# Kernel optimization log

Hardware: AMD Instinct MI355X
Metric: run time of the kernel (lower is better)

Reference implementation:

```python
import jax, jax.numpy as jnp
import numpy as np

H = 512      # config.hidden_dim
N = 64       # batch
W = 512      # sentence length
K = 8        # decode steps = pointer_answers.size(1)
NEG_BIG = 1e10


def setup_inputs() -> dict:
    key = jax.random.key(0)
    ks = jax.random.split(key, 10)
    stdv = 1.0 / np.sqrt(H)
    u = lambda k_, shape, s: jax.random.uniform(k_, shape, jnp.float32, -s, s)
    return {
        "context": jax.random.normal(ks[0], (N, W, 2 * H), jnp.float32),
        "sentence_lens": jax.random.randint(ks[1], (N,), 1, W + 1),
        "pointer_answers": jax.random.randint(ks[2], (N, K), 0, W + 1),
        "V_w": u(ks[3], (H, 2 * H), 1.0 / np.sqrt(2 * H)),
        "W_w": u(ks[4], (H, H), stdv),
        "v": u(ks[5], (H,), stdv),
        "w_ih": u(ks[6], (3 * H, 2 * H), stdv),
        "w_hh": u(ks[7], (3 * H, H), stdv),
        "b_ih": u(ks[8], (3 * H,), stdv),
        "b_hh": u(ks[9], (3 * H,), stdv),
    }


def reference(context, sentence_lens, pointer_answers, V_w, W_w, v, w_ih, w_hh, b_ih, b_hh):
    n, w_len, two_h = context.shape
    h_dim = two_h // 2
    k = pointer_answers.shape[1]

    # encoder output permuted to (W, N, 2H)
    ctx = jnp.swapaxes(context, 0, 1)
    # faithful reproduction of: context_new[i] = (1 - (i >= lens+1)*1e10) * context[i]
    pos = jnp.arange(w_len)[:, None]                                  # (W, 1)
    factor = 1.0 - (pos >= sentence_lens[None, :] + 1).astype(context.dtype) * NEG_BIG  # (W, N)
    ctx_masked = ctx * factor[:, :, None]                             # (W, N, 2H)
    # appended zeros row -> (W+1, N, 2H)
    context_new = jnp.concatenate([ctx_masked, jnp.zeros((1, n, two_h), context.dtype)], axis=0)

    ctx_t = jnp.einsum('snd,hd->snh', context_new, V_w)               # (W+1, N, H) = V(context_new)

    h0 = jnp.zeros((n, h_dim), context.dtype)

    def step(h, _):
        f = jnp.tanh(ctx_t + (h @ W_w.T)[None])                       # (W+1, N, H)
        scores = jnp.einsum('snh,h->sn', f, v)                        # (W+1, N)
        beta = jax.nn.softmax(scores, axis=0)                         # softmax over positions
        aligned = jnp.einsum('sn,snd->nd', beta, context_new)         # (N, 2H)
        # torch GRUCell math
        gi = aligned @ w_ih.T + b_ih                                  # (N, 3H)
        gh = h @ w_hh.T + b_hh                                        # (N, 3H)
        ir, iz, inew = jnp.split(gi, 3, axis=1)
        hr, hz, hnew = jnp.split(gh, 3, axis=1)
        r = jax.nn.sigmoid(ir + hr)
        z = jax.nn.sigmoid(iz + hz)
        ncand = jnp.tanh(inew + r * hnew)
        h_new = (1.0 - z) * ncand + z * h
        return h_new, beta.T                                          # (N, W+1)

    _, betas = jax.lax.scan(step, h0, None, length=k)                 # (k, N, W+1)
    # torch: cat over steps then permute -> (N, k, W+1) -> (N*k, W+1)
    out = jnp.transpose(betas, (1, 0, 2)).reshape(n * k, w_len + 1)
    return out
```

## Files before the change

### kernel.cpp

```cpp
#include <hip/hip_runtime.h>

#define N_    64
#define W_    512
#define H_    512
#define S_    513
#define TWOH_ 1024
#define KS_   8
#define FIXCAP_ 131072

typedef short s16x8 __attribute__((ext_vector_type(8)));
typedef float f32x4 __attribute__((ext_vector_type(4)));
typedef _Float16 h16x8 __attribute__((ext_vector_type(8)));
typedef _Float16 h16x4 __attribute__((ext_vector_type(4)));

__device__ __forceinline__ float tanh_fast(float x) {
  float xc = fminf(fmaxf(x, -15.0f), 15.0f);
  float e = __expf(2.0f * xc);
  return (e - 1.0f) / (e + 1.0f);
}
__device__ __forceinline__ float sigmoid_f(float x) {
  return 1.0f / (1.0f + __expf(-x));
}
__device__ __forceinline__ float wred_sum(float v) {
#pragma unroll
  for (int m = 32; m > 0; m >>= 1) v += __shfl_xor(v, m, 64);
  return v;
}
__device__ __forceinline__ float bf2f(unsigned short u) {
  return __uint_as_float(((unsigned)u) << 16);
}

__device__ __forceinline__ void gld_lds16(const void* g, void* s) {
  __builtin_amdgcn_global_load_lds((__attribute__((address_space(1))) void*)g,
                                   (__attribute__((address_space(3))) void*)s,
                                   16, 0, 0);
}

__global__ __launch_bounds__(256) void k_cvt2(
    const float4* __restrict__ xa, unsigned short* __restrict__ Ahi,
    unsigned short* __restrict__ Alo, const float4* __restrict__ xb,
    unsigned short* __restrict__ Bhi, unsigned short* __restrict__ Blo,
    const float4* __restrict__ xw, _Float16* __restrict__ W16) {
  const int NA = 8388608;
  const int NB = 131072;
  const int NW = 65536;
  const int NT = NA + NB + NW;
  for (int i = blockIdx.x * 256 + threadIdx.x; i < NT; i += gridDim.x * 256) {
    if (i < NA + NB) {
      bool isA = (i < NA);
      float4 v = isA ? xa[i] : xb[i - NA];
      float vs[4] = {v.x, v.y, v.z, v.w};
      unsigned short hb[4], lb[4];
#pragma unroll
      for (int j = 0; j < 4; ++j) {
        unsigned u = __float_as_uint(vs[j]);
        unsigned short h = (unsigned short)((u + 0x7FFFu + ((u >> 16) & 1u)) >> 16);
        float hf = __uint_as_float((unsigned)h << 16);
        float lf = vs[j] - hf;
        unsigned u2 = __float_as_uint(lf);
        unsigned short l = (unsigned short)((u2 + 0x7FFFu + ((u2 >> 16) & 1u)) >> 16);
        hb[j] = h; lb[j] = l;
      }
      ushort4 h4; h4.x = hb[0]; h4.y = hb[1]; h4.z = hb[2]; h4.w = hb[3];
      ushort4 l4; l4.x = lb[0]; l4.y = lb[1]; l4.z = lb[2]; l4.w = lb[3];
      if (isA) {
        ((ushort4*)Ahi)[i] = h4;
        ((ushort4*)Alo)[i] = l4;
      } else {
        ((ushort4*)Bhi)[i - NA] = h4;
        ((ushort4*)Blo)[i - NA] = l4;
      }
    } else {
      int j = i - NA - NB;
      float4 v = xw[j];
      h16x4 o;
      o[0] = (_Float16)v.x; o[1] = (_Float16)v.y;
      o[2] = (_Float16)v.z; o[3] = (_Float16)v.w;
      *(h16x4*)(W16 + (size_t)4 * j) = o;
    }
  }
}

__global__ __launch_bounds__(256, 2) void mfma_gemm(
    const unsigned short* __restrict__ Ahi, const unsigned short* __restrict__ Alo,
    const unsigned short* __restrict__ Bhi, const unsigned short* __restrict__ Blo,
    _Float16* __restrict__ C) {
  __shared__ unsigned short sAh[4096], sAl[4096], sBh[4096], sBl[4096];
  int bid = blockIdx.x;
  int swz = (bid & 7) * 128 + (bid >> 3);
  int mt = swz >> 2, nt = swz & 3;
  int m0 = mt * 128, n0 = nt * 128;
  int tid = threadIdx.x;
  int wave = tid >> 6, lane = tid & 63;
  int wr = wave >> 1, wc = wave & 1;
  int fr = lane & 15, fq = lane >> 4;
  int rA = tid >> 2;
  int cA = (tid & 3) * 8;

  f32x4 acc[4][4] = {};

  const size_t a_row0 = (size_t)(m0 + rA) << 10;
  const size_t a_row1 = (size_t)(m0 + rA + 64) << 10;
  const size_t b_row0 = (size_t)(n0 + rA) << 10;
  const size_t b_row1 = (size_t)(n0 + rA + 64) << 10;
  const int wofs = wave << 9;

  for (int k0 = 0; k0 < 1024; k0 += 32) {
    int off = k0 + cA;
    gld_lds16(Ahi + a_row0 + off, sAh + wofs);
    gld_lds16(Ahi + a_row1 + off, sAh + 2048 + wofs);
    gld_lds16(Alo + a_row0 + off, sAl + wofs);
    gld_lds16(Alo + a_row1 + off, sAl + 2048 + wofs);
    gld_lds16(Bhi + b_row0 + off, sBh + wofs);
    gld_lds16(Bhi + b_row1 + off, sBh + 2048 + wofs);
    gld_lds16(Blo + b_row0 + off, sBl + wofs);
    gld_lds16(Blo + b_row1 + off, sBl + 2048 + wofs);
    __syncthreads();
    s16x8 ah[4], av[4], bh[4], bv[4];
#pragma unroll
    for (int m = 0; m < 4; ++m) {
      int ar = (wr * 64 + m * 16 + fr) * 32 + fq * 8;
      ah[m] = *(const s16x8*)(sAh + ar);
      av[m] = *(const s16x8*)(sAl + ar);
    }
#pragma unroll
    for (int n = 0; n < 4; ++n) {
      int br = (wc * 64 + n * 16 + fr) * 32 + fq * 8;
      bh[n] = *(const s16x8*)(sBh + br);
      bv[n] = *(const s16x8*)(sBl + br);
    }
#pragma unroll
    for (int m = 0; m < 4; ++m)
#pragma unroll
      for (int n = 0; n < 4; ++n) {
        acc[m][n] = __builtin_amdgcn_mfma_f32_16x16x32_bf16(ah[m], bh[n], acc[m][n], 0, 0, 0);
        acc[m][n] = __builtin_amdgcn_mfma_f32_16x16x32_bf16(ah[m], bv[n], acc[m][n], 0, 0, 0);
        acc[m][n] = __builtin_amdgcn_mfma_f32_16x16x32_bf16(av[m], bh[n], acc[m][n], 0, 0, 0);
      }
    __syncthreads();
  }
#pragma unroll
  for (int m = 0; m < 4; ++m) {
    int gr0 = m0 + wr * 64 + m * 16 + fq * 4;
#pragma unroll
    for (int n = 0; n < 4; ++n) {
      int gc = n0 + wc * 64 + n * 16 + fr;
      _Float16* cp = C + (size_t)gr0 * 512 + gc;
#pragma unroll
      for (int r = 0; r < 4; ++r) cp[(size_t)r * 512] = (_Float16)acc[m][n][r];
    }
  }
}

__global__ __launch_bounds__(1024) void k_mscore(
    const int* __restrict__ slens, const float* __restrict__ vvec,
    const _Float16* __restrict__ Vc16, float* __restrict__ scores,
    int* __restrict__ fixcnt, int* __restrict__ fixlist) {
  int nb = blockIdx.x & 63, cb = blockIdx.x >> 6;
  int t = threadIdx.x;
  int len = slens[nb];
  int w = t >> 6, lane = t & 63;
  int hb = lane << 3;
  float4 v0 = *(const float4*)(vvec + hb);
  float4 v1 = *(const float4*)(vvec + hb + 4);
  float vv[8] = {v0.x, v0.y, v0.z, v0.w, v1.x, v1.y, v1.z, v1.w};
  int s0 = max(cb * 128, len + 1);
  int s_end = min((cb + 1) * 128, W_);
  for (int s = s0 + w; s < s_end; s += 16) {
    h16x8 x8 = *(const h16x8*)(Vc16 + ((size_t)nb * W_ + s) * H_ + hb);
    float acc = 0.0f;
#pragma unroll
    for (int i = 0; i < 8; ++i) {
      float vcv = (float)x8[i];
      if (fabsf(vcv) < 6e-5f) {
        int idx = atomicAdd(fixcnt, 1);
        if (idx < FIXCAP_) fixlist[idx] = (nb << 20) | (s << 10) | (hb + i);
      } else {
        acc += (vcv > 0.0f) ? -vv[i] : vv[i];
      }
    }
    acc = wred_sum(acc);
    if (lane == 0) scores[nb * S_ + s] = acc;
  }
}

__global__ __launch_bounds__(256) void k_fix(
    const float* __restrict__ ctx, const float* __restrict__ Vw,
    const float* __restrict__ vvec, const int* __restrict__ fixcnt,
    const int* __restrict__ fixlist, float* __restrict__ scores) {
  int wid = (blockIdx.x * 256 + threadIdx.x) >> 6;
  int lane = threadIdx.x & 63;
  int cnt = min(*fixcnt, FIXCAP_);
  for (int e = wid; e < cnt; e += 1024) {
    int pk = fixlist[e];
    int n = pk >> 20, s = (pk >> 10) & 1023, h = pk & 1023;
    const float* cr = ctx + ((size_t)n * W_ + s) * TWOH_ + lane * 16;
    const float* wr = Vw + (size_t)h * TWOH_ + lane * 16;
    double acc = 0.0;
#pragma unroll
    for (int i = 0; i < 16; ++i) acc += (double)cr[i] * (double)wr[i];
#pragma unroll
    for (int m = 32; m > 0; m >>= 1) acc += __shfl_xor(acc, m, 64);
    if (lane == 0) {
      float vh = vvec[h];
      float contrib = (acc > 0.0) ? -vh : ((acc < 0.0) ? vh : 0.0f);
      if (contrib != 0.0f) atomicAdd(&scores[n * S_ + s], contrib);
    }
  }
}

__global__ __launch_bounds__(1024) void k_prep2(
    const float* __restrict__ ctx, const int* __restrict__ slens,
    const float* __restrict__ scores, float* __restrict__ Cmask) {
  __shared__ float4 red4[16 * 64];
  int nb = blockIdx.x & 63, cb = blockIdx.x >> 6;
  int t = threadIdx.x;
  int len = slens[nb];
  int dl = t & 63, sl = t >> 6;
  int d4 = cb * 256 + dl * 4;
  const float4* cp = (const float4*)(ctx + (size_t)nb * W_ * TWOH_) + (d4 >> 2);
  float4 acc = make_float4(0.f, 0.f, 0.f, 0.f);
#pragma unroll 4
  for (int s = len + 1 + sl; s < W_; s += 16) {
    float ew = __expf(scores[nb * S_ + s]);
    float4 c4 = cp[(size_t)s * (TWOH_ / 4)];
    acc.x += ew * c4.x; acc.y += ew * c4.y;
    acc.z += ew * c4.z; acc.w += ew * c4.w;
  }
  red4[sl * 64 + dl] = acc;
  __syncthreads();
  if (sl == 0) {
    float4 s4 = red4[dl];
#pragma unroll
    for (int i = 1; i < 16; ++i) {
      float4 o = red4[i * 64 + dl];
      s4.x += o.x; s4.y += o.y; s4.z += o.z; s4.w += o.w;
    }
    s4.x *= -1.0e10f; s4.y *= -1.0e10f; s4.z *= -1.0e10f; s4.w *= -1.0e10f;
    *(float4*)(Cmask + nb * TWOH_ + d4) = s4;
  }
}

__global__ __launch_bounds__(1024) void k_scores_hw(
    const int* __restrict__ slens, const float* __restrict__ hc,
    const _Float16* __restrict__ W16, const _Float16* __restrict__ Vc16,
    const float* __restrict__ vvec, float* __restrict__ scores, int k) {
  __shared__ float s_hW[512];
  int nb = blockIdx.x & 63, cb = blockIdx.x >> 6;
  int t = threadIdx.x;
  int w = t >> 6, lane = t & 63;
  int hb = lane << 3;

  if (k == 0) {
    if (t < 512) s_hW[t] = 0.0f;
  } else {
    float4 ha = *(const float4*)(hc + (size_t)nb * H_ + hb);
    float4 hbv = *(const float4*)(hc + (size_t)nb * H_ + hb + 4);
    float hx[8] = {ha.x, ha.y, ha.z, ha.w, hbv.x, hbv.y, hbv.z, hbv.w};
    for (int o = w; o < 512; o += 16) {
      h16x8 w8 = *(const h16x8*)(W16 + (size_t)o * H_ + hb);
      float a = 0.0f;
#pragma unroll
      for (int i = 0; i < 8; ++i) a += hx[i] * (float)w8[i];
      a = wred_sum(a);
      if (lane == 0) s_hW[o] = a;
    }
  }
  __syncthreads();

  int len = slens[nb];
  int smax = min(len, W_ - 1);
  float4 h0 = *(const float4*)(s_hW + hb);
  float4 h1 = *(const float4*)(s_hW + hb + 4);
  float4 v0 = *(const float4*)(vvec + hb);
  float4 v1 = *(const float4*)(vvec + hb + 4);
  float hw[8] = {h0.x, h0.y, h0.z, h0.w, h1.x, h1.y, h1.z, h1.w};
  float vv[8] = {v0.x, v0.y, v0.z, v0.w, v1.x, v1.y, v1.z, v1.w};
  int s_end = min((cb + 1) * 128 - 1, smax);
  const _Float16* vcb = Vc16 + (size_t)nb * W_ * H_ + hb;
  int s = cb * 128 + w;
  for (; s + 48 <= s_end; s += 64) {
    h16x8 x0 = *(const h16x8*)(vcb + (size_t)s * H_);
    h16x8 x1 = *(const h16x8*)(vcb + (size_t)(s + 16) * H_);
    h16x8 x2 = *(const h16x8*)(vcb + (size_t)(s + 32) * H_);
    h16x8 x3 = *(const h16x8*)(vcb + (size_t)(s + 48) * H_);
    float a0 = 0.f, a1 = 0.f, a2 = 0.f, a3 = 0.f;
#pragma unroll
    for (int i = 0; i < 8; ++i) {
      a0 += tanh_fast((float)x0[i] + hw[i]) * vv[i];
      a1 += tanh_fast((float)x1[i] + hw[i]) * vv[i];
      a2 += tanh_fast((float)x2[i] + hw[i]) * vv[i];
      a3 += tanh_fast((float)x3[i] + hw[i]) * vv[i];
    }
    a0 = wred_sum(a0); a1 = wred_sum(a1);
    a2 = wred_sum(a2); a3 = wred_sum(a3);
    if (lane == 0) {
      scores[nb * S_ + s] = a0;
      scores[nb * S_ + s + 16] = a1;
      scores[nb * S_ + s + 32] = a2;
      scores[nb * S_ + s + 48] = a3;
    }
  }
  for (; s <= s_end; s += 16) {
    h16x8 x8 = *(const h16x8*)(vcb + (size_t)s * H_);
    float acc = 0.0f;
#pragma unroll
    for (int i = 0; i < 8; ++i) acc += tanh_fast((float)x8[i] + hw[i]) * vv[i];
    acc = wred_sum(acc);
    if (lane == 0) scores[nb * S_ + s] = acc;
  }
  if (cb == 3 && w == 15) {
    float acc = 0.0f;
#pragma unroll
    for (int i = 0; i < 8; ++i) acc += tanh_fast(hw[i]) * vv[i];
    acc = wred_sum(acc);
    if (lane == 0) scores[nb * S_ + W_] = acc;
  }
}

__global__ __launch_bounds__(1024) void k_soft_aligned(
    const unsigned short* __restrict__ ctxb, const int* __restrict__ slens,
    const float* __restrict__ scores, const float* __restrict__ Cmask,
    float* __restrict__ alignedb, float* __restrict__ out, int k) {
  __shared__ float beta[520];
  __shared__ float wsum[16];
  __shared__ float redl[64 * 16 * 8];
  int nb = blockIdx.x & 63, cb = blockIdx.x >> 6;
  int t = threadIdx.x;
  int len = slens[nb];
  int smax = min(len, W_ - 1);

  float e = (t < S_) ? __expf(scores[nb * S_ + t]) : 0.0f;
  float ws_ = wred_sum(e);
  if ((t & 63) == 0) wsum[t >> 6] = ws_;
  __syncthreads();
  float D = 0.0f;
#pragma unroll
  for (int i = 0; i < 16; ++i) D += wsum[i];
  if (t < S_) {
    float bt = e / D;
    beta[t] = bt;
    if (cb == 0) out[(size_t)(nb * KS_ + k) * S_ + t] = bt;
  }
  __syncthreads();

  int dl = t & 15, sl = t >> 4;
  int d8 = cb * 128 + dl * 8;
  const unsigned short* cp = ctxb + (size_t)nb * W_ * TWOH_ + d8;
  float a[8] = {};
  int s = sl;
  for (; s + 64 <= smax; s += 128) {
    float b0 = beta[s], b1 = beta[s + 64];
    s16x8 c0 = *(const s16x8*)(cp + (size_t)s * TWOH_);
    s16x8 c1 = *(const s16x8*)(cp + (size_t)(s + 64) * TWOH_);
#pragma unroll
    for (int i = 0; i < 8; ++i)
      a[i] += b0 * bf2f((unsigned short)c0[i]) + b1 * bf2f((unsigned short)c1[i]);
  }
  for (; s <= smax; s += 64) {
    float bt = beta[s];
    s16x8 c = *(const s16x8*)(cp + (size_t)s * TWOH_);
#pragma unroll
    for (int i = 0; i < 8; ++i) a[i] += bt * bf2f((unsigned short)c[i]);
  }
  float4* rp = (float4*)(redl + sl * 128 + dl * 8);
  rp[0] = make_float4(a[0], a[1], a[2], a[3]);
  rp[1] = make_float4(a[4], a[5], a[6], a[7]);
  __syncthreads();
  if (t < 128) {
    float ssum = 0.0f;
#pragma unroll 16
    for (int q = 0; q < 64; ++q) ssum += redl[q * 128 + t];
    float coef = 1.0f / D;
    int dd = nb * TWOH_ + cb * 128 + t;
    alignedb[dd] = ssum + coef * Cmask[dd];
  }
}

__global__ __launch_bounds__(1024) void k_gru(
    const float* __restrict__ alignedb, const float* __restrict__ hc,
    const float* __restrict__ wih, const float* __restrict__ whh,
    const float* __restrict__ bih, const float* __restrict__ bhh,
    float* __restrict__ hnx) {
  __shared__ float ls_wih[6 * TWOH_];
  __shared__ float ls_whh[6 * H_];
  __shared__ float part[8 * 128 * 6];
  int b = blockIdx.x;
  int t = threadIdx.x;
  const int j0 = 2 * b;
  for (int i = t; i < 6 * TWOH_; i += 1024) {
    int row = i >> 10, d = i & 1023;
    int jl = row / 3, g = row - jl * 3;
    ls_wih[i] = wih[(size_t)(g * H_ + j0 + jl) * TWOH_ + d];
  }
  for (int i = t; i < 6 * H_; i += 1024) {
    int row = i >> 9, d = i & 511;
    int jl = row / 3, g = row - jl * 3;
    ls_whh[i] = whh[(size_t)(g * H_ + j0 + jl) * H_ + d];
  }
  __syncthreads();
  int nj = t & 127, sl = t >> 7;
  int n = nj & 63, jl = nj >> 6;
  const float* ar = alignedb + n * TWOH_ + sl * 128;
  const float* hr = hc + n * H_ + sl * 64;
  const float* w0 = ls_wih + (jl * 3 + 0) * TWOH_ + sl * 128;
  const float* w1 = ls_wih + (jl * 3 + 1) * TWOH_ + sl * 128;
  const float* w2 = ls_wih + (jl * 3 + 2) * TWOH_ + sl * 128;
  const float* u0 = ls_whh + (jl * 3 + 0) * H_ + sl * 64;
  const float* u1 = ls_whh + (jl * 3 + 1) * H_ + sl * 64;
  const float* u2 = ls_whh + (jl * 3 + 2) * H_ + sl * 64;
  float g0 = 0.f, g1 = 0.f, g2 = 0.f;
#pragma unroll 8
  for (int i = 0; i < 128; i += 4) {
    float4 a4 = *(const float4*)(ar + i);
    g0 += a4.x * w0[i] + a4.y * w0[i + 1] + a4.z * w0[i + 2] + a4.w * w0[i + 3];
    g1 += a4.x * w1[i] + a4.y * w1[i + 1] + a4.z * w1[i + 2] + a4.w * w1[i + 3];
    g2 += a4.x * w2[i] + a4.y * w2[i + 1] + a4.z * w2[i + 2] + a4.w * w2[i + 3];
  }
  float q0 = 0.f, q1 = 0.f, q2 = 0.f;
#pragma unroll 8
  for (int i = 0; i < 64; i += 4) {
    float4 h4 = *(const float4*)(hr + i);
    q0 += h4.x * u0[i] + h4.y * u0[i + 1] + h4.z * u0[i + 2] + h4.w * u0[i + 3];
    q1 += h4.x * u1[i] + h4.y * u1[i + 1] + h4.z * u1[i + 2] + h4.w * u1[i + 3];
    q2 += h4.x * u2[i] + h4.y * u2[i + 1] + h4.z * u2[i + 2] + h4.w * u2[i + 3];
  }
  float* pp = part + (sl * 128 + nj) * 6;
  pp[0] = g0; pp[1] = g1; pp[2] = g2; pp[3] = q0; pp[4] = q1; pp[5] = q2;
  __syncthreads();
  if (t < 128) {
    int n2 = t & 63, jl2 = t >> 6;
    int j = j0 + jl2;
    float G0 = 0.f, G1 = 0.f, G2 = 0.f, Q0 = 0.f, Q1 = 0.f, Q2 = 0.f;
#pragma unroll
    for (int s = 0; s < 8; ++s) {
      float* p = part + (s * 128 + t) * 6;
      G0 += p[0]; G1 += p[1]; G2 += p[2];
      Q0 += p[3]; Q1 += p[4]; Q2 += p[5];
    }
    float r = sigmoid_f(G0 + bih[j] + Q0 + bhh[j]);
    float z = sigmoid_f(G1 + bih[H_ + j] + Q1 + bhh[H_ + j]);
    float nc = tanh_fast(G2 + bih[2 * H_ + j] + r * (Q2 + bhh[2 * H_ + j]));
    hnx[n2 * H_ + j] = (1.0f - z) * nc + z * hc[n2 * H_ + j];
  }
}

extern "C" void kernel_launch(void* const* d_in, const int* in_sizes, int n_in,
                              void* d_out, int out_size, void* d_ws, size_t ws_size,
                              hipStream_t stream) {
  const float* ctx = (const float*)d_in[0];
  const int* slens = (const int*)d_in[1];
  const float* Vw = (const float*)d_in[3];
  const float* Ww = (const float*)d_in[4];
  const float* vvec = (const float*)d_in[5];
  const float* wih = (const float*)d_in[6];
  const float* whh = (const float*)d_in[7];
  const float* bih = (const float*)d_in[8];
  const float* bhh = (const float*)d_in[9];
  float* out = (float*)d_out;

  char* p = (char*)d_ws;
  _Float16* Vc16 = (_Float16*)p;      p += (size_t)N_ * W_ * H_ * 2;
  float* scores = (float*)p;          p += (size_t)N_ * S_ * 4;
  int* fixcnt = (int*)p;              p += 256;
  int* fixlist = (int*)p;             p += (size_t)FIXCAP_ * 4;
  float* Cm = (float*)p;              p += (size_t)N_ * TWOH_ * 4;
  float* hb = (float*)p;              p += (size_t)2 * N_ * H_ * 4;
  float* al = (float*)p;              p += (size_t)N_ * TWOH_ * 4;
  unsigned short* Ahi = (unsigned short*)p;  p += (size_t)32768 * 1024 * 2;
  unsigned short* Alo = (unsigned short*)p;  p += (size_t)32768 * 1024 * 2;
  unsigned short* Bhi = (unsigned short*)p;  p += (size_t)512 * 1024 * 2;
  unsigned short* Blo = (unsigned short*)p;  p += (size_t)512 * 1024 * 2;
  _Float16* W16 = (_Float16*)p;       p += (size_t)512 * 512 * 2;
  size_t need = (size_t)(p - (char*)d_ws);
  if (ws_size < need) return;

  hipMemsetAsync(hb, 0, (size_t)N_ * H_ * sizeof(float), stream);
  hipMemsetAsync(fixcnt, 0, sizeof(int), stream);
  k_cvt2<<<2048, 256, 0, stream>>>((const float4*)ctx, Ahi, Alo,
                                   (const float4*)Vw, Bhi, Blo,
                                   (const float4*)Ww, W16);
  mfma_gemm<<<1024, 256, 0, stream>>>(Ahi, Alo, Bhi, Blo, Vc16);
  k_mscore<<<256, 1024, 0, stream>>>(slens, vvec, Vc16, scores, fixcnt, fixlist);
  k_fix<<<256, 256, 0, stream>>>(ctx, Vw, vvec, fixcnt, fixlist, scores);
  k_prep2<<<256, 1024, 0, stream>>>(ctx, slens, scores, Cm);

  for (int k = 0; k < KS_; ++k) {
    const float* hc = hb + (k & 1) * (N_ * H_);
    float* hn = hb + ((k + 1) & 1) * (N_ * H_);
    k_scores_hw<<<256, 1024, 0, stream>>>(slens, hc, W16, Vc16, vvec, scores, k);
    k_soft_aligned<<<512, 1024, 0, stream>>>(Ahi, slens, scores, Cm, al, out, k);
    k_gru<<<256, 1024, 0, stream>>>(al, hc, wih, whh, bih, bhh, hn);
  }
}
```

Measured before the change: 704.4 us.

## Fuse per-step score and softmax-aligned kernels into one block per batch row

Merges the score computation and the softmax/weighted-context kernels into a single kernel with one 1024-thread block per batch element. Scores stay in shared memory instead of going through global memory, and one launch per decode step is removed. In exchange the grid drops from 256 and 512 blocks to 64, which leaves most compute units idle on a large GPU. The h·W product is no longer recomputed in four blocks per row.

```diff
diff --git a/kernel.cpp b/kernel.cpp
--- a/kernel.cpp
+++ b/kernel.cpp
@@ -241,21 +241,29 @@
   }
 }
 
-__global__ __launch_bounds__(1024) void k_scores_hw(
+__global__ __launch_bounds__(1024) void k_step(
     const int* __restrict__ slens, const float* __restrict__ hc,
     const _Float16* __restrict__ W16, const _Float16* __restrict__ Vc16,
-    const float* __restrict__ vvec, float* __restrict__ scores, int k) {
+    const float* __restrict__ vvec, const float* __restrict__ scores_g,
+    const float* __restrict__ Cmask, const unsigned short* __restrict__ ctxb,
+    float* __restrict__ alignedb, float* __restrict__ out, int k) {
   __shared__ float s_hW[512];
-  int nb = blockIdx.x & 63, cb = blockIdx.x >> 6;
-  int t = threadIdx.x;
-  int w = t >> 6, lane = t & 63;
-  int hb = lane << 3;
+  __shared__ float s_sc[520];
+  __shared__ float beta[520];
+  __shared__ float wsum[16];
+  __shared__ float redl[8 * 128 * 8];
+  const int n = blockIdx.x;
+  const int t = threadIdx.x;
+  const int w = t >> 6, lane = t & 63;
+  const int hb = lane << 3;
+  const int len = slens[n];
+  const int smax = min(len, W_ - 1);
 
   if (k == 0) {
     if (t < 512) s_hW[t] = 0.0f;
   } else {
-    float4 ha = *(const float4*)(hc + (size_t)nb * H_ + hb);
-    float4 hbv = *(const float4*)(hc + (size_t)nb * H_ + hb + 4);
+    float4 ha = *(const float4*)(hc + (size_t)n * H_ + hb);
+    float4 hbv = *(const float4*)(hc + (size_t)n * H_ + hb + 4);
     float hx[8] = {ha.x, ha.y, ha.z, ha.w, hbv.x, hbv.y, hbv.z, hbv.w};
     for (int o = w; o < 512; o += 16) {
       h16x8 w8 = *(const h16x8*)(W16 + (size_t)o * H_ + hb);
@@ -266,20 +274,19 @@
       if (lane == 0) s_hW[o] = a;
     }
   }
-  __syncthreads();
-
-  int len = slens[nb];
-  int smax = min(len, W_ - 1);
+  for (int i = t; i < 512; i += 1024)
+    if (i > smax) s_sc[i] = scores_g[n * S_ + i];
+  __syncthreads();
+
   float4 h0 = *(const float4*)(s_hW + hb);
   float4 h1 = *(const float4*)(s_hW + hb + 4);
   float4 v0 = *(const float4*)(vvec + hb);
   float4 v1 = *(const float4*)(vvec + hb + 4);
   float hw[8] = {h0.x, h0.y, h0.z, h0.w, h1.x, h1.y, h1.z, h1.w};
   float vv[8] = {v0.x, v0.y, v0.z, v0.w, v1.x, v1.y, v1.z, v1.w};
-  int s_end = min((cb + 1) * 128 - 1, smax);
-  const _Float16* vcb = Vc16 + (size_t)nb * W_ * H_ + hb;
-  int s = cb * 128 + w;
-  for (; s + 48 <= s_end; s += 64) {
+  const _Float16* vcb = Vc16 + (size_t)n * W_ * H_ + hb;
+  int s = w;
+  for (; s + 48 <= smax; s += 64) {
     h16x8 x0 = *(const h16x8*)(vcb + (size_t)s * H_);
     h16x8 x1 = *(const h16x8*)(vcb + (size_t)(s + 16) * H_);
     h16x8 x2 = *(const h16x8*)(vcb + (size_t)(s + 32) * H_);
@@ -295,44 +302,30 @@
     a0 = wred_sum(a0); a1 = wred_sum(a1);
     a2 = wred_sum(a2); a3 = wred_sum(a3);
     if (lane == 0) {
-      scores[nb * S_ + s] = a0;
-      scores[nb * S_ + s + 16] = a1;
-      scores[nb * S_ + s + 32] = a2;
-      scores[nb * S_ + s + 48] = a3;
-    }
-  }
-  for (; s <= s_end; s += 16) {
+      s_sc[s] = a0; s_sc[s + 16] = a1;
+      s_sc[s + 32] = a2; s_sc[s + 48] = a3;
+    }
+  }
+  for (; s <= smax; s += 16) {
     h16x8 x8 = *(const h16x8*)(vcb + (size_t)s * H_);
     float acc = 0.0f;
 #pragma unroll
     for (int i = 0; i < 8; ++i) acc += tanh_fast((float)x8[i] + hw[i]) * vv[i];
     acc = wred_sum(acc);
-    if (lane == 0) scores[nb * S_ + s] = acc;
-  }
-  if (cb == 3 && w == 15) {
+    if (lane == 0) s_sc[s] = acc;
+  }
+  if (w == 15) {
     float acc = 0.0f;
 #pragma unroll
     for (int i = 0; i < 8; ++i) acc += tanh_fast(hw[i]) * vv[i];
     acc = wred_sum(acc);
-    if (lane == 0) scores[nb * S_ + W_] = acc;
-  }
-}
-
-__global__ __launch_bounds__(1024) void k_soft_aligned(
-    const unsigned short* __restrict__ ctxb, const int* __restrict__ slens,
-    const float* __restrict__ scores, const float* __restrict__ Cmask,
-    float* __restrict__ alignedb, float* __restrict__ out, int k) {
-  __shared__ float beta[520];
-  __shared__ float wsum[16];
-  __shared__ float redl[64 * 16 * 8];
-  int nb = blockIdx.x & 63, cb = blockIdx.x >> 6;
-  int t = threadIdx.x;
-  int len = slens[nb];
-  int smax = min(len, W_ - 1);
-
-  float e = (t < S_) ? __expf(scores[nb * S_ + t]) : 0.0f;
+    if (lane == 0) s_sc[W_] = acc;
+  }
+  __syncthreads();
+
+  float e = (t < S_) ? __expf(s_sc[t]) : 0.0f;
   float ws_ = wred_sum(e);
-  if ((t & 63) == 0) wsum[t >> 6] = ws_;
+  if (lane == 0) wsum[w] = ws_;
   __syncthreads();
   float D = 0.0f;
 #pragma unroll
@@ -340,40 +333,39 @@
   if (t < S_) {
     float bt = e / D;
     beta[t] = bt;
-    if (cb == 0) out[(size_t)(nb * KS_ + k) * S_ + t] = bt;
-  }
-  __syncthreads();
-
-  int dl = t & 15, sl = t >> 4;
-  int d8 = cb * 128 + dl * 8;
-  const unsigned short* cp = ctxb + (size_t)nb * W_ * TWOH_ + d8;
+    out[(size_t)(n * KS_ + k) * S_ + t] = bt;
+  }
+  __syncthreads();
+
+  int dg = t & 127, sl = t >> 7;
+  int d8 = dg * 8;
+  const unsigned short* cp = ctxb + (size_t)n * W_ * TWOH_ + d8;
   float a[8] = {};
-  int s = sl;
-  for (; s + 64 <= smax; s += 128) {
-    float b0 = beta[s], b1 = beta[s + 64];
+  s = sl;
+  for (; s + 8 <= smax; s += 16) {
+    float b0 = beta[s], b1 = beta[s + 8];
     s16x8 c0 = *(const s16x8*)(cp + (size_t)s * TWOH_);
-    s16x8 c1 = *(const s16x8*)(cp + (size_t)(s + 64) * TWOH_);
+    s16x8 c1 = *(const s16x8*)(cp + (size_t)(s + 8) * TWOH_);
 #pragma unroll
     for (int i = 0; i < 8; ++i)
       a[i] += b0 * bf2f((unsigned short)c0[i]) + b1 * bf2f((unsigned short)c1[i]);
   }
-  for (; s <= smax; s += 64) {
+  for (; s <= smax; s += 8) {
     float bt = beta[s];
     s16x8 c = *(const s16x8*)(cp + (size_t)s * TWOH_);
 #pragma unroll
     for (int i = 0; i < 8; ++i) a[i] += bt * bf2f((unsigned short)c[i]);
   }
-  float4* rp = (float4*)(redl + sl * 128 + dl * 8);
+  float4* rp = (float4*)(redl + sl * 1024 + d8);
   rp[0] = make_float4(a[0], a[1], a[2], a[3]);
   rp[1] = make_float4(a[4], a[5], a[6], a[7]);
   __syncthreads();
-  if (t < 128) {
+  {
     float ssum = 0.0f;
-#pragma unroll 16
-    for (int q = 0; q < 64; ++q) ssum += redl[q * 128 + t];
+#pragma unroll
+    for (int q = 0; q < 8; ++q) ssum += redl[q * 1024 + t];
     float coef = 1.0f / D;
-    int dd = nb * TWOH_ + cb * 128 + t;
-    alignedb[dd] = ssum + coef * Cmask[dd];
+    alignedb[n * TWOH_ + t] = ssum + coef * Cmask[n * TWOH_ + t];
   }
 }
 
@@ -488,8 +480,8 @@
   for (int k = 0; k < KS_; ++k) {
     const float* hc = hb + (k & 1) * (N_ * H_);
     float* hn = hb + ((k + 1) & 1) * (N_ * H_);
-    k_scores_hw<<<256, 1024, 0, stream>>>(slens, hc, W16, Vc16, vvec, scores, k);
-    k_soft_aligned<<<512, 1024, 0, stream>>>(Ahi, slens, scores, Cm, al, out, k);
+    k_step<<<64, 1024, 0, stream>>>(slens, hc, W16, Vc16, vvec, scores, Cm,
+                                    Ahi, al, out, k);
     k_gru<<<256, 1024, 0, stream>>>(al, hc, wih, whh, bih, bhh, hn);
   }
 }
```

Result: slower. 979.7 us (+39.1%).
